# Kernel optimization log

Measured on AMD Instinct MI355X. Metric: run time of the kernel, lower is better.

## Reference

```python
import jax, jax.numpy as jnp
import numpy as np

NH, HD = 4, 32  # num_heads, head_dim (embed 128)
EPS = 1e-5


def _ln(x, w):
    # weight-only LayerNorm (xlstm LayerNorm, bias=False)
    mu = jnp.mean(x, axis=-1, keepdims=True)
    var = jnp.var(x, axis=-1, keepdims=True)
    return (x - mu) * jax.lax.rsqrt(var + EPS) * w


def _mh_ln(y, w):
    # MultiHeadLayerNorm: normalize per head over head_dim, weight only
    # y: [B,S,NH,HD], w: [NH,HD]
    mu = jnp.mean(y, axis=-1, keepdims=True)
    var = jnp.var(y, axis=-1, keepdims=True)
    return (y - mu) * jax.lax.rsqrt(var + EPS) * w


def _slstm_scan(gates, R, b):
    # gates: [B,S,4,NH,HD] input-projected (i,f,z,o) preactivations
    # R: [NH,HD,4,HD] per-head recurrent kernel, b: [4,NH,HD] cell bias
    B = gates.shape[0]
    dt = gates.dtype

    def step(carry, g):
        y, c, n, m = carry  # each [B,NH,HD]
        Ry = jnp.einsum("bhd,hdgk->bghk", y, R)  # [B,4,NH,HD]
        raw = g + Ry + b
        iraw, fraw, zraw, oraw = raw[:, 0], raw[:, 1], raw[:, 2], raw[:, 3]
        logfplusm = m + jax.nn.log_sigmoid(fraw)
        # first step (n==0) uses iraw; afterwards stabilized max (exp gating)
        mnew = jnp.where(n == 0.0, iraw, jnp.maximum(iraw, logfplusm))
        ogate = jax.nn.sigmoid(oraw)
        igate = jnp.exp(iraw - mnew)
        fgate = jnp.exp(logfplusm - mnew)
        cnew = fgate * c + igate * jnp.tanh(zraw)
        nnew = fgate * n + igate
        ynew = ogate * cnew / nnew
        return (ynew, cnew, nnew, mnew), ynew

    init = tuple(jnp.zeros((B, NH, HD), dt) for _ in range(4))
    _, ys = jax.lax.scan(step, init, jnp.moveaxis(gates, 1, 0))
    return jnp.moveaxis(ys, 0, 1)  # [B,S,NH,HD]


def _forward(x, w_in, b_in, ln1_w, wg, rk, b_cell, gn_w, ln2_w,
             ffn_up_w, ffn_down_w, post_w, w_out, b_out):
    h = x @ w_in + b_in  # [B,S,E]
    B, S, E = h.shape
    n_blocks = wg.shape[0]
    for i in range(n_blocks):
        # --- sLSTM sub-block (pre-norm residual) ---
        hn = _ln(h, ln1_w[i]).reshape(B, S, NH, HD)
        # block-diagonal headwise gate projections (i,f,z,o), bias-free
        gates = jnp.einsum("bshd,ghod->bsgho", hn, wg[i])  # [B,S,4,NH,HD]
        y = _slstm_scan(gates, rk[i], b_cell[i])  # [B,S,NH,HD]
        y = _mh_ln(y, gn_w[i].reshape(NH, HD)).reshape(B, S, E)
        h = h + y  # dropout disabled (eval)
        # --- gated FFN sub-block (proj_factor=1.0, gelu) ---
        hn2 = _ln(h, ln2_w[i])
        up = hn2 @ ffn_up_w[i]  # [B,S,2E]
        gate, upv = jnp.split(up, 2, axis=-1)
        h = h + (jax.nn.gelu(gate, approximate=False) * upv) @ ffn_down_w[i]
    h = _ln(h, post_w)
    out = h[:, -1] @ w_out + b_out  # [B,1]
    return out.squeeze(-1)  # [B]


def setup_inputs() -> dict:
    key = jax.random.key(0)
    ks = jax.random.split(key, 10)
    B, S, D, E, NB = 4096, 64, 3, 128, 2

    def rn(k, shape, scale):
        return jax.random.normal(k, shape, dtype=jnp.float32) * scale

    return {
        "x": jax.random.normal(ks[0], (B, S, D), dtype=jnp.float32),
        "w_in": rn(ks[1], (D, E), 0.5),
        "b_in": rn(ks[2], (E,), 0.1),
        "ln1_w": jnp.ones((NB, E), jnp.float32),
        "wg": rn(ks[3], (NB, 4, NH, HD, HD), 0.15),
        "rk": rn(ks[4], (NB, NH, HD, 4, HD), 0.15),
        "b_cell": rn(ks[5], (NB, 4, NH, HD), 0.1),
        "gn_w": jnp.ones((NB, E), jnp.float32),
        "ln2_w": jnp.ones((NB, E), jnp.float32),
        "ffn_up_w": rn(ks[6], (NB, E, 2 * E), 0.1),
        "ffn_down_w": rn(ks[7], (NB, E, E), 0.1),
        "post_w": jnp.ones((E,), jnp.float32),
        "w_out": rn(ks[8], (E, 1), 0.1),
        "b_out": jnp.zeros((1,), jnp.float32),
    }


def reference(x, w_in, b_in, ln1_w, wg, rk, b_cell, gn_w, ln2_w,
              ffn_up_w, ffn_down_w, post_w, w_out, b_out):
    return _forward(x, w_in, b_in, ln1_w, wg, rk, b_cell, gn_w, ln2_w,
                    ffn_up_w, ffn_down_w, post_w, w_out, b_out)
```

## Files before the change

### kernel.cpp

```cpp
#include <hip/hip_runtime.h>
#include <math.h>

#define Bc 4096
#define NHc 4
#define HDc 32
#define Ec 128
#define Sc 64
#define EPSc 1e-5f

using bf16x8 = __attribute__((ext_vector_type(8))) short;
using f32x4  = __attribute__((ext_vector_type(4))) float;

#define MFMA(a,b,c) __builtin_amdgcn_mfma_f32_16x16x32_bf16((a),(b),(c),0,0,0)
#define RCP(x) __builtin_amdgcn_rcpf(x)

__device__ __forceinline__ short f2bf(float f) {
  union { float f; unsigned u; } v; v.f = f;
  unsigned r = v.u + 0x7fffu + ((v.u >> 16) & 1u);
  return (short)(r >> 16);
}
__device__ __forceinline__ float bf2f(short s) {
  union { unsigned u; float f; } v; v.u = ((unsigned)(unsigned short)s) << 16;
  return v.f;
}

__device__ __forceinline__ float gelu_exact(float g) {
  float x  = g * 0.70710678118654752f;
  float ax = fabsf(x);
  float t  = RCP(1.f + 0.3275911f*ax);
  float y  = t*(0.254829592f + t*(-0.284496736f + t*(1.421413741f
           + t*(-1.453152027f + t*1.061405429f))));
  float e  = __expf(-ax*ax);
  float er = 1.f - y*e;
  er = (x < 0.f) ? -er : er;
  return 0.5f*g*(1.f + er);
}

__global__ __launch_bounds__(256) void k_init_h(const float* __restrict__ x,
    const float* __restrict__ w_in, const float* __restrict__ b_in,
    float* __restrict__ h, int total) {
  int idx = blockIdx.x * 256 + threadIdx.x;
  if (idx >= total) return;
  int e = idx & 127;
  int bs = idx >> 7;
  float v = b_in[e] + x[bs*3]*w_in[e] + x[bs*3+1]*w_in[128+e] + x[bs*3+2]*w_in[256+e];
  h[idx] = v;
}

__global__ void k_prep_w(const float* __restrict__ wg, const float* __restrict__ rk,
    const float* __restrict__ wup, const float* __restrict__ wdn,
    short* __restrict__ wch, short* __restrict__ wcl,
    short* __restrict__ wuph, short* __restrict__ wupl,
    short* __restrict__ wdnh, short* __restrict__ wdnl) {
  int ib = blockIdx.x;
  int tid = threadIdx.x;
  const float* wgp = wg + ib*16384;
  const float* rkp = rk + ib*16384;
  for (int idx = tid; idx < 32768; idx += 256) {
    int j = idx & 7, lane = (idx>>3)&63, kf = (idx>>9)&1, nt = (idx>>10)&7, hh = idx>>13;
    int n = nt*16 + (lane&15); int g = n>>5, o = n&31;
    int k = kf*32 + (lane>>4)*8 + j;
    float v = (k < 32) ? wgp[((g*NHc+hh)*HDc + o)*HDc + k]
                       : rkp[((hh*HDc + (k-32))*4 + g)*HDc + o];
    short hi16 = f2bf(v);
    wch[ib*32768 + idx] = hi16;
    wcl[ib*32768 + idx] = f2bf(v - bf2f(hi16));
  }
  const float* wupp = wup + ib*32768;
  for (int idx = tid; idx < 32768; idx += 256) {
    int j = idx&7, lane=(idx>>3)&63, kf=(idx>>9)&3, nt = idx>>11;
    int n = nt*16 + (lane&15); int k = kf*32 + (lane>>4)*8 + j;
    float v = wupp[k*256 + n];
    short hi16 = f2bf(v);
    wuph[ib*32768 + idx] = hi16;
    wupl[ib*32768 + idx] = f2bf(v - bf2f(hi16));
  }
  const float* wdnp = wdn + ib*16384;
  for (int idx = tid; idx < 16384; idx += 256) {
    int j = idx&7, lane=(idx>>3)&63, kf=(idx>>9)&3, nt = idx>>11;
    int n = nt*16+(lane&15); int k = kf*32+(lane>>4)*8+j;
    float v = wdnp[k*128 + n];
    short hi16 = f2bf(v);
    wdnh[ib*16384 + idx] = hi16;
    wdnl[ib*16384 + idx] = f2bf(v - bf2f(hi16));
  }
}

__global__ __launch_bounds__(512, 2) void k_scan4(float* __restrict__ h,
    const short* __restrict__ wch, const short* __restrict__ wcl,
    const float* __restrict__ bcell, const float* __restrict__ ln1w,
    const float* __restrict__ gnw) {
  __shared__ short ybh[2][4][16][40];
  __shared__ short ybl[2][4][16][40];
  __shared__ float LNp[2][4][16][2];
  const int tid = threadIdx.x;
  const int wid = tid >> 6;
  const int hh = wid >> 1;
  const int p  = wid & 1;
  const int lane = tid & 63;
  const int l15 = lane & 15, hi = lane >> 4;
  const int bg = blockIdx.x;

  bf16x8 Bh[4][2], Bl[4][2];
  #pragma unroll
  for (int i = 0; i < 4; i++)
    #pragma unroll
    for (int kf = 0; kf < 2; kf++) {
      int off = ((hh*16 + (2*i+p)*2 + kf)*64 + lane)*8;
      Bh[i][kf] = *(const bf16x8*)(wch + off);
      Bl[i][kf] = *(const bf16x8*)(wcl + off);
    }

  float biasv[4];
  #pragma unroll
  for (int i = 0; i < 4; i++)
    biasv[i] = bcell[(i*NHc + hh)*HDc + p*16 + l15];
  float lnw[8], gwv[8];
  #pragma unroll
  for (int j = 0; j < 8; j++) {
    lnw[j] = ln1w[hh*32 + hi*8 + j];
    gwv[j] = gnw[hh*32 + hi*8 + j];
  }

  for (int i = tid; i < 4*16*40; i += 512) {
    ybh[1][0][0][i] = 0; ybl[1][0][0][i] = 0;
  }

  float cs[4], ns[4], ms[4];
  #pragma unroll
  for (int r = 0; r < 4; r++) { cs[r]=0.f; ns[r]=0.f; ms[r]=0.f; }

  float* hbase = h + ((size_t)(bg*16 + l15)*Sc)*Ec + hh*32 + hi*8;
  float4 ha = *(const float4*)(hbase);
  float4 hb = *(const float4*)(hbase + 4);
  float hvprev[8];

  __syncthreads();

  for (int s = 0; s < Sc; s++) {
    float hv[8];
    *(float4*)&hv[0] = ha; *(float4*)&hv[4] = hb;
    if (s < 63) {
      ha = *(const float4*)(hbase + (s+1)*Ec);
      hb = *(const float4*)(hbase + (s+1)*Ec + 4);
    }
    float sum = 0.f, sq = 0.f;
    #pragma unroll
    for (int j = 0; j < 8; j++) { sum += hv[j]; sq += hv[j]*hv[j]; }
    sum += __shfl_xor(sum, 16); sq += __shfl_xor(sq, 16);
    sum += __shfl_xor(sum, 32); sq += __shfl_xor(sq, 32);
    if (p == 0 && hi == 0) { LNp[s&1][hh][l15][0] = sum; LNp[s&1][hh][l15][1] = sq; }
    __syncthreads();
    float tsum = LNp[s&1][0][l15][0] + LNp[s&1][1][l15][0]
               + LNp[s&1][2][l15][0] + LNp[s&1][3][l15][0];
    float tsq  = LNp[s&1][0][l15][1] + LNp[s&1][1][l15][1]
               + LNp[s&1][2][l15][1] + LNp[s&1][3][l15][1];
    float mu = tsum * (1.f/128.f);
    float rs = rsqrtf(tsq*(1.f/128.f) - mu*mu + EPSc);

    bf16x8 Ah, Al;
    #pragma unroll
    for (int j = 0; j < 8; j++) {
      float hn = (hv[j]-mu)*rs*lnw[j];
      short h16 = f2bf(hn);
      Ah[j] = h16;
      Al[j] = f2bf(hn - bf2f(h16));
    }
    const int sbY = (s&1)^1;
    bf16x8 Yh = *(const bf16x8*)&ybh[sbY][hh][l15][hi*8];
    bf16x8 Yl = *(const bf16x8*)&ybl[sbY][hh][l15][hi*8];

    if (s && p == 0) {
      float y8[8], s2 = 0.f, q2 = 0.f;
      #pragma unroll
      for (int j = 0; j < 8; j++) {
        y8[j] = bf2f(Yh[j]) + bf2f(Yl[j]);
        s2 += y8[j]; q2 += y8[j]*y8[j];
      }
      s2 += __shfl_xor(s2, 16); q2 += __shfl_xor(q2, 16);
      s2 += __shfl_xor(s2, 32); q2 += __shfl_xor(q2, 32);
      float mu2 = s2 * (1.f/32.f);
      float rs2 = rsqrtf(q2*(1.f/32.f) - mu2*mu2 + EPSc);
      float4 o0, o1;
      o0.x = hvprev[0] + (y8[0]-mu2)*rs2*gwv[0];
      o0.y = hvprev[1] + (y8[1]-mu2)*rs2*gwv[1];
      o0.z = hvprev[2] + (y8[2]-mu2)*rs2*gwv[2];
      o0.w = hvprev[3] + (y8[3]-mu2)*rs2*gwv[3];
      o1.x = hvprev[4] + (y8[4]-mu2)*rs2*gwv[4];
      o1.y = hvprev[5] + (y8[5]-mu2)*rs2*gwv[5];
      o1.z = hvprev[6] + (y8[6]-mu2)*rs2*gwv[6];
      o1.w = hvprev[7] + (y8[7]-mu2)*rs2*gwv[7];
      *(float4*)(hbase + (size_t)(s-1)*Ec)     = o0;
      *(float4*)(hbase + (size_t)(s-1)*Ec + 4) = o1;
    }
    #pragma unroll
    for (int j = 0; j < 8; j++) hvprev[j] = hv[j];

    f32x4 acc[4];
    #pragma unroll
    for (int i = 0; i < 4; i++) {
      f32x4 c; c[0]=biasv[i]; c[1]=biasv[i]; c[2]=biasv[i]; c[3]=biasv[i];
      c = MFMA(Ah, Bh[i][0], c);
      c = MFMA(Ah, Bl[i][0], c);
      c = MFMA(Al, Bh[i][0], c);
      c = MFMA(Yh, Bh[i][1], c);
      c = MFMA(Yh, Bl[i][1], c);
      acc[i] = MFMA(Yl, Bh[i][1], c);
    }

    #pragma unroll
    for (int r = 0; r < 4; r++) {
      float iraw = acc[0][r];
      float fraw = acc[1][r];
      float zraw = acc[2][r];
      float oraw = acc[3][r];
      float ax  = fabsf(fraw);
      float lsg = fminf(fraw, 0.f) - __logf(1.f + __expf(-ax));
      float lfm = ms[r] + lsg;
      float mnew = (ns[r] == 0.f) ? iraw : fmaxf(iraw, lfm);
      float og = RCP(1.f + __expf(-oraw));
      float ig = __expf(iraw - mnew);
      float fg = __expf(lfm - mnew);
      float e2 = __expf(2.f*zraw);
      float th = 1.f - 2.f*RCP(e2 + 1.f);
      float cn = fg*cs[r] + ig*th;
      float nn = fg*ns[r] + ig;
      cs[r] = cn; ns[r] = nn; ms[r] = mnew;
      float y = og*cn*RCP(nn);
      short y16 = f2bf(y);
      ybh[s&1][hh][hi*4+r][p*16+l15] = y16;
      ybl[s&1][hh][hi*4+r][p*16+l15] = f2bf(y - bf2f(y16));
    }
  }

  __syncthreads();
  if (p == 0) {
    bf16x8 Yh = *(const bf16x8*)&ybh[(Sc-1)&1][hh][l15][hi*8];
    bf16x8 Yl = *(const bf16x8*)&ybl[(Sc-1)&1][hh][l15][hi*8];
    float y8[8], s2 = 0.f, q2 = 0.f;
    #pragma unroll
    for (int j = 0; j < 8; j++) {
      y8[j] = bf2f(Yh[j]) + bf2f(Yl[j]);
      s2 += y8[j]; q2 += y8[j]*y8[j];
    }
    s2 += __shfl_xor(s2, 16); q2 += __shfl_xor(q2, 16);
    s2 += __shfl_xor(s2, 32); q2 += __shfl_xor(q2, 32);
    float mu2 = s2 * (1.f/32.f);
    float rs2 = rsqrtf(q2*(1.f/32.f) - mu2*mu2 + EPSc);
    float4 o0, o1;
    o0.x = hvprev[0] + (y8[0]-mu2)*rs2*gwv[0];
    o0.y = hvprev[1] + (y8[1]-mu2)*rs2*gwv[1];
    o0.z = hvprev[2] + (y8[2]-mu2)*rs2*gwv[2];
    o0.w = hvprev[3] + (y8[3]-mu2)*rs2*gwv[3];
    o1.x = hvprev[4] + (y8[4]-mu2)*rs2*gwv[4];
    o1.y = hvprev[5] + (y8[5]-mu2)*rs2*gwv[5];
    o1.z = hvprev[6] + (y8[6]-mu2)*rs2*gwv[6];
    o1.w = hvprev[7] + (y8[7]-mu2)*rs2*gwv[7];
    *(float4*)(hbase + (size_t)(Sc-1)*Ec)     = o0;
    *(float4*)(hbase + (size_t)(Sc-1)*Ec + 4) = o1;
  }
}

__global__ __launch_bounds__(256) void k_ffn4(float* __restrict__ h,
    const float* __restrict__ ln2w,
    const short* __restrict__ wuph, const short* __restrict__ wupl,
    const short* __restrict__ wdnh, const short* __restrict__ wdnl) {
  __shared__ short bufH[8192];
  __shared__ short bufL[8192];
  size_t tok0 = (size_t)blockIdx.x * 64;
  int tid = threadIdx.x;
  int wv = tid >> 6, lane = tid & 63, l15 = lane & 15, hi = lane >> 4;

  {
    int t = tid >> 2, sub = tid & 3;
    const float* row = h + (tok0 + t)*Ec + sub*32;
    float v[32];
    #pragma unroll
    for (int q = 0; q < 8; q++) *(float4*)&v[q*4] = *(const float4*)&row[q*4];
    float sum = 0.f, sq = 0.f;
    #pragma unroll
    for (int j = 0; j < 32; j++) { sum += v[j]; sq += v[j]*v[j]; }
    sum += __shfl_xor(sum,1); sq += __shfl_xor(sq,1);
    sum += __shfl_xor(sum,2); sq += __shfl_xor(sq,2);
    float mu = sum * (1.f/128.f);
    float rs = rsqrtf(sq*(1.f/128.f) - mu*mu + EPSc);
    #pragma unroll
    for (int q2 = 0; q2 < 4; q2++) {
      bf16x8 ph, pl;
      #pragma unroll
      for (int j = 0; j < 8; j++) {
        float hn = (v[q2*8+j]-mu)*rs*ln2w[sub*32+q2*8+j];
        short h16 = f2bf(hn);
        ph[j] = h16;
        pl[j] = f2bf(hn - bf2f(h16));
      }
      int byte = (t*256 + sub*64 + q2*16) ^ ((t&7)<<4);
      *(bf16x8*)((char*)bufH + byte) = ph;
      *(bf16x8*)((char*)bufL + byte) = pl;
    }
  }
  __syncthreads();

  f32x4 ag[2][4], au[2][4];
  #pragma unroll
  for (int p = 0; p < 2; p++)
    #pragma unroll
    for (int mt = 0; mt < 4; mt++)
      #pragma unroll
      for (int r = 0; r < 4; r++) { ag[p][mt][r]=0.f; au[p][mt][r]=0.f; }
  #pragma unroll 1
  for (int kf = 0; kf < 4; kf++) {
    bf16x8 Ah[4], Al[4];
    #pragma unroll
    for (int mt = 0; mt < 4; mt++) {
      int rw = mt*16 + l15;
      int byte = (rw*256 + kf*64 + hi*16) ^ ((rw&7)<<4);
      Ah[mt] = *(const bf16x8*)((const char*)bufH + byte);
      Al[mt] = *(const bf16x8*)((const char*)bufL + byte);
    }
    #pragma unroll
    for (int p = 0; p < 2; p++) {
      int gOff = (((2*wv+p)*4 + kf)*64 + lane)*8;
      int uOff = (((8+2*wv+p)*4 + kf)*64 + lane)*8;
      bf16x8 Bgh = *(const bf16x8*)(wuph + gOff);
      bf16x8 Bgl = *(const bf16x8*)(wupl + gOff);
      bf16x8 Buh = *(const bf16x8*)(wuph + uOff);
      bf16x8 Bul = *(const bf16x8*)(wupl + uOff);
      #pragma unroll
      for (int mt = 0; mt < 4; mt++) {
        ag[p][mt] = MFMA(Ah[mt], Bgh, ag[p][mt]);
        ag[p][mt] = MFMA(Ah[mt], Bgl, ag[p][mt]);
        ag[p][mt] = MFMA(Al[mt], Bgh, ag[p][mt]);
        au[p][mt] = MFMA(Ah[mt], Buh, au[p][mt]);
        au[p][mt] = MFMA(Ah[mt], Bul, au[p][mt]);
        au[p][mt] = MFMA(Al[mt], Buh, au[p][mt]);
      }
    }
  }
  __syncthreads();
  #pragma unroll
  for (int p = 0; p < 2; p++)
    #pragma unroll
    for (int mt = 0; mt < 4; mt++)
      #pragma unroll
      for (int r = 0; r < 4; r++) {
        float g = ag[p][mt][r], u = au[p][mt][r];
        float a = gelu_exact(g)*u;
        int m = mt*16 + hi*4 + r, f = (2*wv+p)*16 + l15;
        int byte = (m*256 + f*2) ^ ((m&7)<<4);
        short a16 = f2bf(a);
        *(short*)((char*)bufH + byte) = a16;
        *(short*)((char*)bufL + byte) = f2bf(a - bf2f(a16));
      }
  __syncthreads();

  f32x4 oc[2][4];
  #pragma unroll
  for (int p = 0; p < 2; p++)
    #pragma unroll
    for (int mt = 0; mt < 4; mt++)
      #pragma unroll
      for (int r = 0; r < 4; r++) oc[p][mt][r] = 0.f;
  #pragma unroll 1
  for (int kf = 0; kf < 4; kf++) {
    bf16x8 Ah[4], Al[4];
    #pragma unroll
    for (int mt = 0; mt < 4; mt++) {
      int rw = mt*16 + l15;
      int byte = (rw*256 + kf*64 + hi*16) ^ ((rw&7)<<4);
      Ah[mt] = *(const bf16x8*)((const char*)bufH + byte);
      Al[mt] = *(const bf16x8*)((const char*)bufL + byte);
    }
    #pragma unroll
    for (int p = 0; p < 2; p++) {
      int dOff = (((2*wv+p)*4 + kf)*64 + lane)*8;
      bf16x8 Bdh = *(const bf16x8*)(wdnh + dOff);
      bf16x8 Bdl = *(const bf16x8*)(wdnl + dOff);
      #pragma unroll
      for (int mt = 0; mt < 4; mt++) {
        oc[p][mt] = MFMA(Ah[mt], Bdh, oc[p][mt]);
        oc[p][mt] = MFMA(Ah[mt], Bdl, oc[p][mt]);
        oc[p][mt] = MFMA(Al[mt], Bdh, oc[p][mt]);
      }
    }
  }
  #pragma unroll
  for (int p = 0; p < 2; p++)
    #pragma unroll
    for (int mt = 0; mt < 4; mt++)
      #pragma unroll
      for (int r = 0; r < 4; r++) {
        int m = mt*16 + hi*4 + r, e = (2*wv+p)*16 + l15;
        float* hp = h + (tok0 + m)*Ec + e;
        *hp += oc[p][mt][r];
      }
}

__global__ __launch_bounds__(256) void k_out(const float* __restrict__ h,
    const float* __restrict__ postw, const float* __restrict__ wout,
    const float* __restrict__ bout, float* __restrict__ out, int B) {
  int gw = (blockIdx.x * blockDim.x + threadIdx.x) >> 6;
  int lane = threadIdx.x & 63;
  if (gw >= B) return;
  const float* row = h + ((size_t)gw*Sc + (Sc-1))*Ec;
  float v0 = row[lane], v1 = row[64+lane];
  float sum = v0+v1, sq = v0*v0+v1*v1;
  #pragma unroll
  for (int m = 1; m < 64; m <<= 1) { sum += __shfl_xor(sum, m); sq += __shfl_xor(sq, m); }
  float mu = sum * (1.f/128.f);
  float rs = rsqrtf(sq*(1.f/128.f) - mu*mu + EPSc);
  float d = (v0-mu)*rs*postw[lane]*wout[lane] + (v1-mu)*rs*postw[64+lane]*wout[64+lane];
  #pragma unroll
  for (int m = 1; m < 64; m <<= 1) d += __shfl_xor(d, m);
  if (lane == 0) out[gw] = d + bout[0];
}

extern "C" void kernel_launch(void* const* d_in, const int* in_sizes, int n_in,
                              void* d_out, int out_size, void* d_ws, size_t ws_size,
                              hipStream_t stream) {
  const float* x     = (const float*)d_in[0];
  const float* w_in  = (const float*)d_in[1];
  const float* b_in  = (const float*)d_in[2];
  const float* ln1_w = (const float*)d_in[3];
  const float* wg    = (const float*)d_in[4];
  const float* rk    = (const float*)d_in[5];
  const float* bcell = (const float*)d_in[6];
  const float* gn_w  = (const float*)d_in[7];
  const float* ln2_w = (const float*)d_in[8];
  const float* wup   = (const float*)d_in[9];
  const float* wdn   = (const float*)d_in[10];
  const float* postw = (const float*)d_in[11];
  const float* w_out = (const float*)d_in[12];
  const float* b_out = (const float*)d_in[13];
  float* out = (float*)d_out;

  char* p = (char*)d_ws;
  float* h    = (float*)p;            p += 134217728;
  short* wch  = (short*)p;            p += 131072;
  short* wcl  = (short*)p;            p += 131072;
  short* wuph = (short*)p;            p += 131072;
  short* wupl = (short*)p;            p += 131072;
  short* wdnh = (short*)p;            p += 65536;
  short* wdnl = (short*)p;            p += 65536;

  k_prep_w<<<2, 256, 0, stream>>>(wg, rk, wup, wdn, wch, wcl,
                                  wuph, wupl, wdnh, wdnl);
  k_init_h<<<(Bc*Sc*Ec)/256, 256, 0, stream>>>(x, w_in, b_in, h, Bc*Sc*Ec);
  for (int ib = 0; ib < 2; ib++) {
    k_scan4<<<Bc/16, 512, 0, stream>>>(h, wch + ib*32768, wcl + ib*32768,
                                       bcell + ib*512, ln1_w + ib*128, gn_w + ib*128);
    k_ffn4<<<(Bc*Sc)/64, 256, 0, stream>>>(h, ln2_w + ib*128,
                                           wuph + ib*32768, wupl + ib*32768,
                                           wdnh + ib*16384, wdnl + ib*16384);
  }
  k_out<<<Bc/4, 256, 0, stream>>>(h, postw, w_out, b_out, out, Bc);
}
```

Before: 615.2 us.

## Fuse input projection into first scan kernel and alternate residual writers

Removes the separate kernel that materialized h = x@w_in + b_in and instead computes it on the fly inside the first sLSTM scan launch from x, which avoids writing and re-reading the 128MB h buffer once. The residual/group-norm write-back now alternates between the two wave halves by step parity to balance work. It also adds the lo*lo MFMA terms for both the input and recurrent products, raising MFMA count per step from 6 to 8 for accuracy at extra compute cost.

```diff
diff --git a/kernel.cpp b/kernel.cpp
--- a/kernel.cpp
+++ b/kernel.cpp
@@ -34,17 +34,6 @@
   float er = 1.f - y*e;
   er = (x < 0.f) ? -er : er;
   return 0.5f*g*(1.f + er);
-}
-
-__global__ __launch_bounds__(256) void k_init_h(const float* __restrict__ x,
-    const float* __restrict__ w_in, const float* __restrict__ b_in,
-    float* __restrict__ h, int total) {
-  int idx = blockIdx.x * 256 + threadIdx.x;
-  if (idx >= total) return;
-  int e = idx & 127;
-  int bs = idx >> 7;
-  float v = b_in[e] + x[bs*3]*w_in[e] + x[bs*3+1]*w_in[128+e] + x[bs*3+2]*w_in[256+e];
-  h[idx] = v;
 }
 
 __global__ void k_prep_w(const float* __restrict__ wg, const float* __restrict__ rk,
@@ -86,10 +75,12 @@
   }
 }
 
-__global__ __launch_bounds__(512, 2) void k_scan4(float* __restrict__ h,
+__global__ __launch_bounds__(512, 2) void k_scan6(float* __restrict__ h,
+    const float* __restrict__ x, const float* __restrict__ w_in,
+    const float* __restrict__ b_in,
     const short* __restrict__ wch, const short* __restrict__ wcl,
     const float* __restrict__ bcell, const float* __restrict__ ln1w,
-    const float* __restrict__ gnw) {
+    const float* __restrict__ gnw, int first) {
   __shared__ short ybh[2][4][16][40];
   __shared__ short ybl[2][4][16][40];
   __shared__ float LNp[2][4][16][2];
@@ -121,6 +112,15 @@
     lnw[j] = ln1w[hh*32 + hi*8 + j];
     gwv[j] = gnw[hh*32 + hi*8 + j];
   }
+  float wv0[8], wv1[8], wv2[8], bi[8];
+  if (first) {
+    #pragma unroll
+    for (int j = 0; j < 8; j++) {
+      int col = hh*32 + hi*8 + j;
+      wv0[j] = w_in[col]; wv1[j] = w_in[128+col]; wv2[j] = w_in[256+col];
+      bi[j] = b_in[col];
+    }
+  }
 
   for (int i = tid; i < 4*16*40; i += 512) {
     ybh[1][0][0][i] = 0; ybl[1][0][0][i] = 0;
@@ -131,18 +131,34 @@
   for (int r = 0; r < 4; r++) { cs[r]=0.f; ns[r]=0.f; ms[r]=0.f; }
 
   float* hbase = h + ((size_t)(bg*16 + l15)*Sc)*Ec + hh*32 + hi*8;
-  float4 ha = *(const float4*)(hbase);
-  float4 hb = *(const float4*)(hbase + 4);
+  const float* xbase = x + ((size_t)(bg*16 + l15)*Sc)*3;
+  float4 ha, hb;
+  float xa0, xa1, xa2;
+  if (first) {
+    xa0 = xbase[0]; xa1 = xbase[1]; xa2 = xbase[2];
+  } else {
+    ha = *(const float4*)(hbase);
+    hb = *(const float4*)(hbase + 4);
+  }
   float hvprev[8];
 
   __syncthreads();
 
   for (int s = 0; s < Sc; s++) {
     float hv[8];
-    *(float4*)&hv[0] = ha; *(float4*)&hv[4] = hb;
-    if (s < 63) {
-      ha = *(const float4*)(hbase + (s+1)*Ec);
-      hb = *(const float4*)(hbase + (s+1)*Ec + 4);
+    if (first) {
+      #pragma unroll
+      for (int j = 0; j < 8; j++)
+        hv[j] = bi[j] + xa0*wv0[j] + xa1*wv1[j] + xa2*wv2[j];
+      if (s < 63) {
+        xa0 = xbase[(s+1)*3]; xa1 = xbase[(s+1)*3+1]; xa2 = xbase[(s+1)*3+2];
+      }
+    } else {
+      *(float4*)&hv[0] = ha; *(float4*)&hv[4] = hb;
+      if (s < 63) {
+        ha = *(const float4*)(hbase + (s+1)*Ec);
+        hb = *(const float4*)(hbase + (s+1)*Ec + 4);
+      }
     }
     float sum = 0.f, sq = 0.f;
     #pragma unroll
@@ -170,7 +186,7 @@
     bf16x8 Yh = *(const bf16x8*)&ybh[sbY][hh][l15][hi*8];
     bf16x8 Yl = *(const bf16x8*)&ybl[sbY][hh][l15][hi*8];
 
-    if (s && p == 0) {
+    if (s && ((s & 1) == p)) {
       float y8[8], s2 = 0.f, q2 = 0.f;
       #pragma unroll
       for (int j = 0; j < 8; j++) {
@@ -203,9 +219,11 @@
       c = MFMA(Ah, Bh[i][0], c);
       c = MFMA(Ah, Bl[i][0], c);
       c = MFMA(Al, Bh[i][0], c);
+      c = MFMA(Al, Bl[i][0], c);
       c = MFMA(Yh, Bh[i][1], c);
       c = MFMA(Yh, Bl[i][1], c);
-      acc[i] = MFMA(Yl, Bh[i][1], c);
+      c = MFMA(Yl, Bh[i][1], c);
+      acc[i] = MFMA(Yl, Bl[i][1], c);
     }
 
     #pragma unroll
@@ -445,10 +463,11 @@
 
   k_prep_w<<<2, 256, 0, stream>>>(wg, rk, wup, wdn, wch, wcl,
                                   wuph, wupl, wdnh, wdnl);
-  k_init_h<<<(Bc*Sc*Ec)/256, 256, 0, stream>>>(x, w_in, b_in, h, Bc*Sc*Ec);
   for (int ib = 0; ib < 2; ib++) {
-    k_scan4<<<Bc/16, 512, 0, stream>>>(h, wch + ib*32768, wcl + ib*32768,
-                                       bcell + ib*512, ln1_w + ib*128, gn_w + ib*128);
+    k_scan6<<<Bc/16, 512, 0, stream>>>(h, x, w_in, b_in,
+                                       wch + ib*32768, wcl + ib*32768,
+                                       bcell + ib*512, ln1_w + ib*128, gn_w + ib*128,
+                                       ib == 0 ? 1 : 0);
     k_ffn4<<<(Bc*Sc)/64, 256, 0, stream>>>(h, ln2_w + ib*128,
                                            wuph + ib*32768, wupl + ib*32768,
                                            wdnh + ib*16384, wdnl + ib*16384);
```

Measured after the change: 580.5 us. -5.7%, faster.
